# Kernel tuning notes

Hardware: AMD Instinct MI355X
Metric: run time of the kernel (lower is better)

Reference implementation:

```python
import jax, jax.numpy as jnp
import numpy as np

ALPHA = 2.0
EPS = 1e-12  # F.normalize default eps


def setup_inputs() -> dict:
    key = jax.random.key(0)
    k1, k2 = jax.random.split(key)
    x = jax.random.normal(k1, (16, 512, 48, 48), dtype=jnp.float32)
    # 1x1 conv weight [out=1, in=C, 1, 1] flattened to [C], xavier-like scale
    w_query = jax.random.normal(k2, (512,), dtype=jnp.float32) * (2.0 / (512 + 1)) ** 0.5
    return {"x": x, "w_query": w_query}


def reference(x, w_query):
    b, c, h, w = x.shape
    n = h * w
    # attention map from detached x: 1x1 conv (dot over channels) + softplus -> [b, n]
    xd = jax.lax.stop_gradient(x)
    att = jax.nn.softplus(jnp.einsum('bchw,c->bhw', xd, w_query)).reshape(b, n)
    # L2-normalize over channel dim, flatten spatial -> [b, c, n]
    norm = jnp.sqrt(jnp.sum(x * x, axis=1, keepdims=True))
    flat = (x / jnp.maximum(norm, EPS)).reshape(b, c, n)
    # full NxN similarity, relu^alpha
    sim = jnp.einsum('bcn,bcm->bnm', flat, flat)  # [b, n, n]
    score = jnp.maximum(sim, 0.0) ** ALPHA
    # combine with attention map -> refine score per spatial location
    refine = jnp.einsum('bnm,bm->bn', score, att).reshape(b, 1, h, w)
    # weighted global average pool -> [b, c, 1, 1]
    return jnp.mean(x * refine, axis=(2, 3), keepdims=True)
```

## Files before the change

### kernel.cpp

```cpp
#include <hip/hip_runtime.h>

#define C_DIM 512
#define N_PIX 2304
#define B_DIM 16
#define K8    (C_DIM / 8)
#define K8_STRIDE (N_PIX * 8)
#define FB_STRIDE ((size_t)K8 * K8_STRIDE)

typedef float floatx4 __attribute__((ext_vector_type(4)));
typedef __bf16 bf16x8 __attribute__((ext_vector_type(8)));

static __device__ __forceinline__ unsigned short f2bf(float f) {
    unsigned u = __float_as_uint(f);
    return (unsigned short)((u + 0x7fffu + ((u >> 16) & 1u)) >> 16);
}

static __device__ __forceinline__ void load_lds16(const void* g, void* l) {
    __builtin_amdgcn_global_load_lds(
        (const __attribute__((address_space(1))) unsigned int*)g,
        (__attribute__((address_space(3))) unsigned int*)l, 16, 0, 0);
}

__global__ __launch_bounds__(256) void prep_convert_kernel(const float* __restrict__ x,
                                                           const float* __restrict__ w,
                                                           float* __restrict__ rnorm,
                                                           float* __restrict__ normb,
                                                           float* __restrict__ att,
                                                           unsigned short* __restrict__ F) {
    const int tid = threadIdx.x;
    const int px = tid & 63;
    const int cc = tid >> 6;
    const int b  = (blockIdx.x * 64) / N_PIX;
    const int p0 = (blockIdx.x * 64) % N_PIX;
    const int p  = p0 + px;

    const float* xb = x + (size_t)b * C_DIM * N_PIX;

    float dot = 0.f, sq = 0.f;
    #pragma unroll 4
    for (int c = cc * 128; c < cc * 128 + 128; ++c) {
        float v = xb[(size_t)c * N_PIX + p];
        dot = fmaf(v, w[c], dot);
        sq  = fmaf(v, v, sq);
    }
    __shared__ float sdot[4][64];
    __shared__ float ssq[4][64];
    __shared__ __align__(16) float srn[64];
    sdot[cc][px] = dot;
    ssq[cc][px]  = sq;
    __syncthreads();
    if (cc == 0) {
        dot = sdot[0][px] + sdot[1][px] + sdot[2][px] + sdot[3][px];
        sq  = ssq[0][px]  + ssq[1][px]  + ssq[2][px]  + ssq[3][px];
        float z = dot;
        float sp = (z > 0.f) ? (z + log1pf(expf(-z))) : log1pf(expf(z));
        att[b * N_PIX + p] = sp;
        float nv = fmaxf(sqrtf(sq), 1e-12f);
        normb[b * N_PIX + p] = nv;
        float rv = 1.0f / nv;
        rnorm[b * N_PIX + p] = rv;
        srn[px] = rv;
    }
    __syncthreads();

    const int n4l = tid & 15;
    const int k8b = tid >> 4;
    const float4 rv4 = *(const float4*)&srn[n4l * 4];
    #pragma unroll
    for (int it = 0; it < 4; ++it) {
        const int k8 = k8b + 16 * it;
        union { unsigned short u[4][8]; int4 v[4]; } cell;
        #pragma unroll
        for (int kk = 0; kk < 8; ++kk) {
            float4 xv = *(const float4*)(xb + (size_t)(k8 * 8 + kk) * N_PIX + p0 + n4l * 4);
            cell.u[0][kk] = f2bf(xv.x * rv4.x);
            cell.u[1][kk] = f2bf(xv.y * rv4.y);
            cell.u[2][kk] = f2bf(xv.z * rv4.z);
            cell.u[3][kk] = f2bf(xv.w * rv4.w);
        }
        unsigned short* dst = F + (size_t)b * FB_STRIDE + (size_t)k8 * K8_STRIDE
                            + (size_t)(p0 + n4l * 4) * 8;
        #pragma unroll
        for (int i = 0; i < 4; ++i)
            *(int4*)(dst + i * 8) = cell.v[i];
    }
}

__global__ __launch_bounds__(256) void refine_kernel(const unsigned short* __restrict__ F,
                                                     const float* __restrict__ att,
                                                     float* __restrict__ refine) {
    const int id   = blockIdx.x;
    const int xcd  = id & 7;
    const int slot = id >> 3;
    const int hi   = (slot >= 171) ? 1 : 0;
    const int b    = xcd + 8 * hi;
    int t = slot - 171 * hi, bi = 0;
    while (t >= 18 - bi) { t -= 18 - bi; ++bi; }
    const int bj = bi + t;
    const int n0 = bi * 128;
    const int m0 = bj * 128;
    const bool mirror = (bi != bj);

    const unsigned short* Fb = F + (size_t)b * FB_STRIDE;
    const float* ab = att + b * N_PIX;

    __shared__ __align__(16) unsigned short As[8 * 128 * 8];
    __shared__ __align__(16) unsigned short Bs[8 * 128 * 8];

    const int tid  = threadIdx.x;
    const int lane = tid & 63;
    const int wave = tid >> 6;
    const int wr = wave >> 1, wc = wave & 1;
    const int quad = lane >> 4, lcol = lane & 15;

    floatx4 acc[4][4];
    #pragma unroll
    for (int i = 0; i < 4; ++i)
        #pragma unroll
        for (int j = 0; j < 4; ++j)
            acc[i][j] = (floatx4)0.f;

    for (int ck = 0; ck < 8; ++ck) {
        __syncthreads();
        #pragma unroll
        for (int h = 0; h < 2; ++h) {
            const int kbl = wave * 2 + h;
            const unsigned short* sA = Fb + (size_t)(ck * 8 + kbl) * K8_STRIDE
                                     + (size_t)n0 * 8 + lane * 8;
            const unsigned short* sB = Fb + (size_t)(ck * 8 + kbl) * K8_STRIDE
                                     + (size_t)m0 * 8 + lane * 8;
            load_lds16(sA,       &As[kbl * 1024]);
            load_lds16(sA + 512, &As[kbl * 1024 + 512]);
            load_lds16(sB,       &Bs[kbl * 1024]);
            load_lds16(sB + 512, &Bs[kbl * 1024 + 512]);
        }
        __syncthreads();

        #pragma unroll
        for (int h = 0; h < 2; ++h) {
            const int kb = h * 4 + quad;
            bf16x8 af[4], bfr[4];
            #pragma unroll
            for (int mi = 0; mi < 4; ++mi)
                af[mi] = *(const bf16x8*)&As[(kb * 128 + wr * 64 + mi * 16 + lcol) * 8];
            #pragma unroll
            for (int ni = 0; ni < 4; ++ni)
                bfr[ni] = *(const bf16x8*)&Bs[(kb * 128 + wc * 64 + ni * 16 + lcol) * 8];
            #pragma unroll
            for (int mi = 0; mi < 4; ++mi)
                #pragma unroll
                for (int ni = 0; ni < 4; ++ni)
                    acc[mi][ni] = __builtin_amdgcn_mfma_f32_16x16x32_bf16(af[mi], bfr[ni], acc[mi][ni], 0, 0, 0);
        }
    }

    float attC[4];
    #pragma unroll
    for (int ni = 0; ni < 4; ++ni)
        attC[ni] = ab[m0 + wc * 64 + ni * 16 + lcol];

    #pragma unroll
    for (int mi = 0; mi < 4; ++mi) {
        float part[4] = {0.f, 0.f, 0.f, 0.f};
        #pragma unroll
        for (int ni = 0; ni < 4; ++ni) {
            #pragma unroll
            for (int r = 0; r < 4; ++r) {
                float s = fmaxf(acc[mi][ni][r], 0.f);
                part[r] = fmaf(s * s, attC[ni], part[r]);
            }
        }
        #pragma unroll
        for (int r = 0; r < 4; ++r) {
            float v = part[r];
            v += __shfl_xor(v, 1);
            v += __shfl_xor(v, 2);
            v += __shfl_xor(v, 4);
            v += __shfl_xor(v, 8);
            if (lcol == 0)
                atomicAdd(&refine[b * N_PIX + n0 + wr * 64 + mi * 16 + quad * 4 + r], v);
        }
    }

    if (mirror) {
        float attR[4][4];
        #pragma unroll
        for (int mi = 0; mi < 4; ++mi)
            #pragma unroll
            for (int r = 0; r < 4; ++r)
                attR[mi][r] = ab[n0 + wr * 64 + mi * 16 + quad * 4 + r];

        #pragma unroll
        for (int ni = 0; ni < 4; ++ni) {
            float msum = 0.f;
            #pragma unroll
            for (int mi = 0; mi < 4; ++mi) {
                #pragma unroll
                for (int r = 0; r < 4; ++r) {
                    float s = fmaxf(acc[mi][ni][r], 0.f);
                    msum = fmaf(s * s, attR[mi][r], msum);
                }
            }
            msum += __shfl_xor(msum, 16);
            msum += __shfl_xor(msum, 32);
            if (quad == 0)
                atomicAdd(&refine[b * N_PIX + m0 + wc * 64 + ni * 16 + lcol], msum);
        }
    }
}

__global__ __launch_bounds__(256) void refine_fallback(const float* __restrict__ x,
                                                       const float* __restrict__ rnorm,
                                                       const float* __restrict__ att,
                                                       float* __restrict__ refine) {
    const int b  = blockIdx.z;
    const int n0 = blockIdx.x * 128;
    const int m0 = blockIdx.y * 128;
    const float* xb = x + (size_t)b * C_DIM * N_PIX;
    const float* rn = rnorm + b * N_PIX;
    const float* ab = att + b * N_PIX;

    __shared__ __align__(16) unsigned short As[4 * 128 * 8];
    __shared__ __align__(16) unsigned short Bs[4 * 128 * 8];

    const int tid  = threadIdx.x;
    const int nl   = tid & 127;
    const int half = tid >> 7;
    const int lane = tid & 63;
    const int wave = tid >> 6;
    const int wr = wave >> 1, wc = wave & 1;
    const int quad = lane >> 4, lcol = lane & 15;

    const float rA = rn[n0 + nl];
    const float rB = rn[m0 + nl];

    floatx4 acc[4][4];
    #pragma unroll
    for (int i = 0; i < 4; ++i)
        #pragma unroll
        for (int j = 0; j < 4; ++j)
            acc[i][j] = (floatx4)0.f;

    for (int k0 = 0; k0 < C_DIM; k0 += 32) {
        const float* xa = xb + (size_t)(k0 + half * 16) * N_PIX;
        union { unsigned short u[16]; int4 v[2]; } ta, tb;
        #pragma unroll
        for (int j = 0; j < 16; ++j) {
            float va = xa[(size_t)j * N_PIX + n0 + nl];
            float vb = xa[(size_t)j * N_PIX + m0 + nl];
            ta.u[j] = f2bf(va * rA);
            tb.u[j] = f2bf(vb * rB);
        }
        __syncthreads();
        *(int4*)&As[((half * 2 + 0) * 128 + nl) * 8] = ta.v[0];
        *(int4*)&As[((half * 2 + 1) * 128 + nl) * 8] = ta.v[1];
        *(int4*)&Bs[((half * 2 + 0) * 128 + nl) * 8] = tb.v[0];
        *(int4*)&Bs[((half * 2 + 1) * 128 + nl) * 8] = tb.v[1];
        __syncthreads();

        bf16x8 af[4], bfr[4];
        #pragma unroll
        for (int mi = 0; mi < 4; ++mi)
            af[mi] = *(const bf16x8*)&As[(quad * 128 + wr * 64 + mi * 16 + lcol) * 8];
        #pragma unroll
        for (int ni = 0; ni < 4; ++ni)
            bfr[ni] = *(const bf16x8*)&Bs[(quad * 128 + wc * 64 + ni * 16 + lcol) * 8];
        #pragma unroll
        for (int mi = 0; mi < 4; ++mi)
            #pragma unroll
            for (int ni = 0; ni < 4; ++ni)
                acc[mi][ni] = __builtin_amdgcn_mfma_f32_16x16x32_bf16(af[mi], bfr[ni], acc[mi][ni], 0, 0, 0);
    }

    float attv[4];
    #pragma unroll
    for (int ni = 0; ni < 4; ++ni)
        attv[ni] = ab[m0 + wc * 64 + ni * 16 + lcol];

    #pragma unroll
    for (int mi = 0; mi < 4; ++mi) {
        float part[4] = {0.f, 0.f, 0.f, 0.f};
        #pragma unroll
        for (int ni = 0; ni < 4; ++ni) {
            #pragma unroll
            for (int r = 0; r < 4; ++r) {
                float s = fmaxf(acc[mi][ni][r], 0.f);
                part[r] = fmaf(s * s, attv[ni], part[r]);
            }
        }
        #pragma unroll
        for (int r = 0; r < 4; ++r) {
            float v = part[r];
            v += __shfl_xor(v, 1);
            v += __shfl_xor(v, 2);
            v += __shfl_xor(v, 4);
            v += __shfl_xor(v, 8);
            if (lcol == 0)
                atomicAdd(&refine[b * N_PIX + n0 + wr * 64 + mi * 16 + quad * 4 + r], v);
        }
    }
}

__global__ __launch_bounds__(256) void pool_kernel(const unsigned short* __restrict__ F,
                                                   const float* __restrict__ refine,
                                                   const float* __restrict__ normb,
                                                   float* __restrict__ out) {
    const int lane = threadIdx.x & 63;
    const int wave = threadIdx.x >> 6;
    const int g = blockIdx.x * 4 + wave;
    const int b = g >> 6;
    const int k8 = g & 63;
    const unsigned short* Fr = F + (size_t)b * FB_STRIDE + (size_t)k8 * K8_STRIDE;
    const float* rf = refine + b * N_PIX;
    const float* nb = normb + b * N_PIX;
    float s[8] = {0.f, 0.f, 0.f, 0.f, 0.f, 0.f, 0.f, 0.f};
    #pragma unroll 4
    for (int j = 0; j < 36; ++j) {
        const int n = j * 64 + lane;
        bf16x8 fv = *(const bf16x8*)(Fr + (size_t)n * 8);
        float rr = rf[n] * nb[n];
        #pragma unroll
        for (int kk = 0; kk < 8; ++kk)
            s[kk] = fmaf((float)fv[kk], rr, s[kk]);
    }
    #pragma unroll
    for (int kk = 0; kk < 8; ++kk) {
        float v = s[kk];
        #pragma unroll
        for (int off = 32; off > 0; off >>= 1) v += __shfl_down(v, off);
        if (lane == 0) out[b * C_DIM + k8 * 8 + kk] = v * (1.0f / N_PIX);
    }
}

__global__ __launch_bounds__(256) void pool_fallback(const float* __restrict__ x,
                                                     const float* __restrict__ refine,
                                                     float* __restrict__ out) {
    const int lane = threadIdx.x & 63;
    const int wave = threadIdx.x >> 6;
    const int g = blockIdx.x * 4 + wave;
    const int b = g >> 9;
    const float4* xr = (const float4*)(x + (size_t)g * N_PIX);
    const float4* rr = (const float4*)(refine + (size_t)b * N_PIX);
    float s = 0.f;
    #pragma unroll
    for (int j = 0; j < 9; ++j) {
        float4 xv = xr[j * 64 + lane];
        float4 rv = rr[j * 64 + lane];
        s += xv.x * rv.x + xv.y * rv.y + xv.z * rv.z + xv.w * rv.w;
    }
    #pragma unroll
    for (int off = 32; off > 0; off >>= 1) s += __shfl_down(s, off);
    if (lane == 0) out[g] = s * (1.0f / N_PIX);
}

__global__ __launch_bounds__(256) void prep_kernel(const float* __restrict__ x,
                                                   const float* __restrict__ w,
                                                   float* __restrict__ rnorm,
                                                   float* __restrict__ normb,
                                                   float* __restrict__ att) {
    const int tid = threadIdx.x;
    const int px = tid & 63;
    const int cc = tid >> 6;
    const int pglob = blockIdx.x * 64 + px;
    const int b = pglob / N_PIX;
    const int p = pglob - b * N_PIX;

    const float* xb = x + (size_t)b * C_DIM * N_PIX + p;
    float dot = 0.f, sq = 0.f;
    #pragma unroll 4
    for (int c = cc * 128; c < cc * 128 + 128; ++c) {
        float v = xb[(size_t)c * N_PIX];
        dot = fmaf(v, w[c], dot);
        sq  = fmaf(v, v, sq);
    }
    __shared__ float sdot[4][64];
    __shared__ float ssq[4][64];
    sdot[cc][px] = dot;
    ssq[cc][px]  = sq;
    __syncthreads();
    if (cc == 0) {
        dot = sdot[0][px] + sdot[1][px] + sdot[2][px] + sdot[3][px];
        sq  = ssq[0][px]  + ssq[1][px]  + ssq[2][px]  + ssq[3][px];
        float z = dot;
        float sp = (z > 0.f) ? (z + log1pf(expf(-z))) : log1pf(expf(z));
        att[pglob] = sp;
        float nv = fmaxf(sqrtf(sq), 1e-12f);
        normb[pglob] = nv;
        rnorm[pglob] = 1.0f / nv;
    }
}

extern "C" void kernel_launch(void* const* d_in, const int* in_sizes, int n_in,
                              void* d_out, int out_size, void* d_ws, size_t ws_size,
                              hipStream_t stream) {
    const float* x = (const float*)d_in[0];
    const float* w = (const float*)d_in[1];
    float* rnorm  = (float*)d_ws;
    float* normb  = rnorm + B_DIM * N_PIX;
    float* att    = normb + B_DIM * N_PIX;
    float* refine = att + B_DIM * N_PIX;
    unsigned short* F = (unsigned short*)(refine + B_DIM * N_PIX);
    float* out    = (float*)d_out;

    const size_t need = (size_t)4 * B_DIM * N_PIX * 4 + (size_t)B_DIM * FB_STRIDE * 2;

    hipMemsetAsync(refine, 0, B_DIM * N_PIX * sizeof(float), stream);
    if (ws_size >= need) {
        prep_convert_kernel<<<dim3(B_DIM * N_PIX / 64), 256, 0, stream>>>(x, w, rnorm, normb, att, F);
        refine_kernel<<<dim3(171 * 16), 256, 0, stream>>>(F, att, refine);
        pool_kernel<<<dim3(B_DIM * K8 / 4), 256, 0, stream>>>(F, refine, normb, out);
    } else {
        prep_kernel<<<dim3(B_DIM * N_PIX / 64), 256, 0, stream>>>(x, w, rnorm, normb, att);
        refine_fallback<<<dim3(18, 18, B_DIM), 256, 0, stream>>>(x, rnorm, att, refine);
        pool_fallback<<<dim3(B_DIM * C_DIM / 4), 256, 0, stream>>>(x, refine, out);
    }
}
```

Measured before the change: 210.8 us.

## Fold normalization into attention weights and fuse prep into a single pass over x

```diff
diff --git a/kernel.cpp b/kernel.cpp
--- a/kernel.cpp
+++ b/kernel.cpp
@@ -15,57 +15,32 @@
     return (unsigned short)((u + 0x7fffu + ((u >> 16) & 1u)) >> 16);
 }
 
-static __device__ __forceinline__ void load_lds16(const void* g, void* l) {
+static __device__ __forceinline__ float softplus_stable(float z) {
+    return (z > 0.f) ? (z + log1pf(expf(-z))) : log1pf(expf(z));
+}
+
+static __device__ __forceinline__ void load_lds16(const void* gp, void* l) {
     __builtin_amdgcn_global_load_lds(
-        (const __attribute__((address_space(1))) unsigned int*)g,
+        (const __attribute__((address_space(1))) unsigned int*)gp,
         (__attribute__((address_space(3))) unsigned int*)l, 16, 0, 0);
 }
 
-__global__ __launch_bounds__(256) void prep_convert_kernel(const float* __restrict__ x,
-                                                           const float* __restrict__ w,
-                                                           float* __restrict__ rnorm,
-                                                           float* __restrict__ normb,
-                                                           float* __restrict__ att,
-                                                           unsigned short* __restrict__ F) {
+__global__ __launch_bounds__(256) void xcvt_kernel(const float* __restrict__ x,
+                                                   const float* __restrict__ w,
+                                                   float* __restrict__ g,
+                                                   float* __restrict__ rn2,
+                                                   float* __restrict__ refine,
+                                                   unsigned short* __restrict__ F) {
     const int tid = threadIdx.x;
-    const int px = tid & 63;
-    const int cc = tid >> 6;
     const int b  = (blockIdx.x * 64) / N_PIX;
     const int p0 = (blockIdx.x * 64) % N_PIX;
-    const int p  = p0 + px;
-
-    const float* xb = x + (size_t)b * C_DIM * N_PIX;
-
-    float dot = 0.f, sq = 0.f;
-    #pragma unroll 4
-    for (int c = cc * 128; c < cc * 128 + 128; ++c) {
-        float v = xb[(size_t)c * N_PIX + p];
-        dot = fmaf(v, w[c], dot);
-        sq  = fmaf(v, v, sq);
-    }
-    __shared__ float sdot[4][64];
-    __shared__ float ssq[4][64];
-    __shared__ __align__(16) float srn[64];
-    sdot[cc][px] = dot;
-    ssq[cc][px]  = sq;
-    __syncthreads();
-    if (cc == 0) {
-        dot = sdot[0][px] + sdot[1][px] + sdot[2][px] + sdot[3][px];
-        sq  = ssq[0][px]  + ssq[1][px]  + ssq[2][px]  + ssq[3][px];
-        float z = dot;
-        float sp = (z > 0.f) ? (z + log1pf(expf(-z))) : log1pf(expf(z));
-        att[b * N_PIX + p] = sp;
-        float nv = fmaxf(sqrtf(sq), 1e-12f);
-        normb[b * N_PIX + p] = nv;
-        float rv = 1.0f / nv;
-        rnorm[b * N_PIX + p] = rv;
-        srn[px] = rv;
-    }
-    __syncthreads();
-
     const int n4l = tid & 15;
     const int k8b = tid >> 4;
-    const float4 rv4 = *(const float4*)&srn[n4l * 4];
+
+    const float* xb = x + (size_t)b * C_DIM * N_PIX;
+    float4 dot4 = {0.f, 0.f, 0.f, 0.f};
+    float4 sq4  = {0.f, 0.f, 0.f, 0.f};
+
     #pragma unroll
     for (int it = 0; it < 4; ++it) {
         const int k8 = k8b + 16 * it;
@@ -73,10 +48,15 @@
         #pragma unroll
         for (int kk = 0; kk < 8; ++kk) {
             float4 xv = *(const float4*)(xb + (size_t)(k8 * 8 + kk) * N_PIX + p0 + n4l * 4);
-            cell.u[0][kk] = f2bf(xv.x * rv4.x);
-            cell.u[1][kk] = f2bf(xv.y * rv4.y);
-            cell.u[2][kk] = f2bf(xv.z * rv4.z);
-            cell.u[3][kk] = f2bf(xv.w * rv4.w);
+            const float wc = w[k8 * 8 + kk];
+            dot4.x = fmaf(xv.x, wc, dot4.x);  sq4.x = fmaf(xv.x, xv.x, sq4.x);
+            dot4.y = fmaf(xv.y, wc, dot4.y);  sq4.y = fmaf(xv.y, xv.y, sq4.y);
+            dot4.z = fmaf(xv.z, wc, dot4.z);  sq4.z = fmaf(xv.z, xv.z, sq4.z);
+            dot4.w = fmaf(xv.w, wc, dot4.w);  sq4.w = fmaf(xv.w, xv.w, sq4.w);
+            cell.u[0][kk] = f2bf(xv.x);
+            cell.u[1][kk] = f2bf(xv.y);
+            cell.u[2][kk] = f2bf(xv.z);
+            cell.u[3][kk] = f2bf(xv.w);
         }
         unsigned short* dst = F + (size_t)b * FB_STRIDE + (size_t)k8 * K8_STRIDE
                             + (size_t)(p0 + n4l * 4) * 8;
@@ -84,10 +64,35 @@
         for (int i = 0; i < 4; ++i)
             *(int4*)(dst + i * 8) = cell.v[i];
     }
+
+    __shared__ float4 sdot[16][16];
+    __shared__ float4 ssq[16][16];
+    sdot[k8b][n4l] = dot4;
+    ssq[k8b][n4l]  = sq4;
+    __syncthreads();
+
+    if (tid < 16) {
+        float4 d = sdot[0][tid], s = ssq[0][tid];
+        #pragma unroll
+        for (int j = 1; j < 16; ++j) {
+            float4 dj = sdot[j][tid], sj = ssq[j][tid];
+            d.x += dj.x; d.y += dj.y; d.z += dj.z; d.w += dj.w;
+            s.x += sj.x; s.y += sj.y; s.z += sj.z; s.w += sj.w;
+        }
+        float4 r2, gv;
+        r2.x = 1.0f / fmaxf(s.x, 1e-24f);  gv.x = softplus_stable(d.x) * r2.x;
+        r2.y = 1.0f / fmaxf(s.y, 1e-24f);  gv.y = softplus_stable(d.y) * r2.y;
+        r2.z = 1.0f / fmaxf(s.z, 1e-24f);  gv.z = softplus_stable(d.z) * r2.z;
+        r2.w = 1.0f / fmaxf(s.w, 1e-24f);  gv.w = softplus_stable(d.w) * r2.w;
+        const int o = b * N_PIX + p0 + tid * 4;
+        *(float4*)(g   + o) = gv;
+        *(float4*)(rn2 + o) = r2;
+        *(float4*)(refine + o) = (float4){0.f, 0.f, 0.f, 0.f};
+    }
 }
 
 __global__ __launch_bounds__(256) void refine_kernel(const unsigned short* __restrict__ F,
-                                                     const float* __restrict__ att,
+                                                     const float* __restrict__ g,
                                                      float* __restrict__ refine) {
     const int id   = blockIdx.x;
     const int xcd  = id & 7;
@@ -102,7 +107,7 @@
     const bool mirror = (bi != bj);
 
     const unsigned short* Fb = F + (size_t)b * FB_STRIDE;
-    const float* ab = att + b * N_PIX;
+    const float* gb = g + b * N_PIX;
 
     __shared__ __align__(16) unsigned short As[8 * 128 * 8];
     __shared__ __align__(16) unsigned short Bs[8 * 128 * 8];
@@ -120,20 +125,25 @@
         for (int j = 0; j < 4; ++j)
             acc[i][j] = (floatx4)0.f;
 
+    const unsigned short* pA = Fb + (size_t)(wave * 2) * K8_STRIDE + (size_t)n0 * 8 + lane * 8;
+    const unsigned short* pB = Fb + (size_t)(wave * 2) * K8_STRIDE + (size_t)m0 * 8 + lane * 8;
+    unsigned short* const lA0 = &As[(wave * 2) * 1024];
+    unsigned short* const lA1 = &As[(wave * 2 + 1) * 1024];
+    unsigned short* const lB0 = &Bs[(wave * 2) * 1024];
+    unsigned short* const lB1 = &Bs[(wave * 2 + 1) * 1024];
+
     for (int ck = 0; ck < 8; ++ck) {
         __syncthreads();
-        #pragma unroll
-        for (int h = 0; h < 2; ++h) {
-            const int kbl = wave * 2 + h;
-            const unsigned short* sA = Fb + (size_t)(ck * 8 + kbl) * K8_STRIDE
-                                     + (size_t)n0 * 8 + lane * 8;
-            const unsigned short* sB = Fb + (size_t)(ck * 8 + kbl) * K8_STRIDE
-                                     + (size_t)m0 * 8 + lane * 8;
-            load_lds16(sA,       &As[kbl * 1024]);
-            load_lds16(sA + 512, &As[kbl * 1024 + 512]);
-            load_lds16(sB,       &Bs[kbl * 1024]);
-            load_lds16(sB + 512, &Bs[kbl * 1024 + 512]);
-        }
+        load_lds16(pA,                    lA0);
+        load_lds16(pA + 512,              lA0 + 512);
+        load_lds16(pA + K8_STRIDE,        lA1);
+        load_lds16(pA + K8_STRIDE + 512,  lA1 + 512);
+        load_lds16(pB,                    lB0);
+        load_lds16(pB + 512,              lB0 + 512);
+        load_lds16(pB + K8_STRIDE,        lB1);
+        load_lds16(pB + K8_STRIDE + 512,  lB1 + 512);
+        pA += 8 * K8_STRIDE;
+        pB += 8 * K8_STRIDE;
         __syncthreads();
 
         #pragma unroll
@@ -154,10 +164,10 @@
         }
     }
 
-    float attC[4];
+    float gC[4];
     #pragma unroll
     for (int ni = 0; ni < 4; ++ni)
-        attC[ni] = ab[m0 + wc * 64 + ni * 16 + lcol];
+        gC[ni] = gb[m0 + wc * 64 + ni * 16 + lcol];
 
     #pragma unroll
     for (int mi = 0; mi < 4; ++mi) {
@@ -167,7 +177,7 @@
             #pragma unroll
             for (int r = 0; r < 4; ++r) {
                 float s = fmaxf(acc[mi][ni][r], 0.f);
-                part[r] = fmaf(s * s, attC[ni], part[r]);
+                part[r] = fmaf(s * s, gC[ni], part[r]);
             }
         }
         #pragma unroll
@@ -183,12 +193,12 @@
     }
 
     if (mirror) {
-        float attR[4][4];
+        float gR[4][4];
         #pragma unroll
         for (int mi = 0; mi < 4; ++mi)
             #pragma unroll
             for (int r = 0; r < 4; ++r)
-                attR[mi][r] = ab[n0 + wr * 64 + mi * 16 + quad * 4 + r];
+                gR[mi][r] = gb[n0 + wr * 64 + mi * 16 + quad * 4 + r];
 
         #pragma unroll
         for (int ni = 0; ni < 4; ++ni) {
@@ -198,7 +208,7 @@
                 #pragma unroll
                 for (int r = 0; r < 4; ++r) {
                     float s = fmaxf(acc[mi][ni][r], 0.f);
-                    msum = fmaf(s * s, attR[mi][r], msum);
+                    msum = fmaf(s * s, gR[mi][r], msum);
                 }
             }
             msum += __shfl_xor(msum, 16);
@@ -206,6 +216,75 @@
             if (quad == 0)
                 atomicAdd(&refine[b * N_PIX + m0 + wc * 64 + ni * 16 + lcol], msum);
         }
+    }
+}
+
+__global__ __launch_bounds__(256) void pool_kernel(const unsigned short* __restrict__ F,
+                                                   const float* __restrict__ refine,
+                                                   const float* __restrict__ rn2,
+                                                   float* __restrict__ out) {
+    const int lane = threadIdx.x & 63;
+    const int wave = threadIdx.x >> 6;
+    const int b  = blockIdx.x >> 6;
+    const int k8 = blockIdx.x & 63;
+    const unsigned short* Fr = F + (size_t)b * FB_STRIDE + (size_t)k8 * K8_STRIDE;
+    const float* rf = refine + b * N_PIX;
+    const float* r2 = rn2 + b * N_PIX;
+    float s[8] = {0.f, 0.f, 0.f, 0.f, 0.f, 0.f, 0.f, 0.f};
+    #pragma unroll
+    for (int j = 0; j < 9; ++j) {
+        const int n = (j * 4 + wave) * 64 + lane;
+        bf16x8 fv = *(const bf16x8*)(Fr + (size_t)n * 8);
+        float rr = rf[n] * r2[n];
+        #pragma unroll
+        for (int kk = 0; kk < 8; ++kk)
+            s[kk] = fmaf((float)fv[kk], rr, s[kk]);
+    }
+    __shared__ float sred[4][8];
+    #pragma unroll
+    for (int kk = 0; kk < 8; ++kk) {
+        float v = s[kk];
+        #pragma unroll
+        for (int off = 32; off > 0; off >>= 1) v += __shfl_down(v, off);
+        if (lane == 0) sred[wave][kk] = v;
+    }
+    __syncthreads();
+    if (threadIdx.x < 8) {
+        const int kk = threadIdx.x;
+        out[b * C_DIM + k8 * 8 + kk] =
+            (sred[0][kk] + sred[1][kk] + sred[2][kk] + sred[3][kk]) * (1.0f / N_PIX);
+    }
+}
+
+__global__ __launch_bounds__(256) void prep_kernel(const float* __restrict__ x,
+                                                   const float* __restrict__ w,
+                                                   float* __restrict__ rnorm,
+                                                   float* __restrict__ att) {
+    const int tid = threadIdx.x;
+    const int px = tid & 63;
+    const int cc = tid >> 6;
+    const int pglob = blockIdx.x * 64 + px;
+    const int b = pglob / N_PIX;
+    const int p = pglob - b * N_PIX;
+
+    const float* xb = x + (size_t)b * C_DIM * N_PIX + p;
+    float dot = 0.f, sq = 0.f;
+    #pragma unroll 4
+    for (int c = cc * 128; c < cc * 128 + 128; ++c) {
+        float v = xb[(size_t)c * N_PIX];
+        dot = fmaf(v, w[c], dot);
+        sq  = fmaf(v, v, sq);
+    }
+    __shared__ float sdot[4][64];
+    __shared__ float ssq[4][64];
+    sdot[cc][px] = dot;
+    ssq[cc][px]  = sq;
+    __syncthreads();
+    if (cc == 0) {
+        dot = sdot[0][px] + sdot[1][px] + sdot[2][px] + sdot[3][px];
+        sq  = ssq[0][px]  + ssq[1][px]  + ssq[2][px]  + ssq[3][px];
+        att[pglob] = softplus_stable(dot);
+        rnorm[pglob] = 1.0f / fmaxf(sqrtf(sq), 1e-12f);
     }
 }
 
@@ -301,45 +380,14 @@
     }
 }
 
-__global__ __launch_bounds__(256) void pool_kernel(const unsigned short* __restrict__ F,
-                                                   const float* __restrict__ refine,
-                                                   const float* __restrict__ normb,
-                                                   float* __restrict__ out) {
-    const int lane = threadIdx.x & 63;
-    const int wave = threadIdx.x >> 6;
-    const int g = blockIdx.x * 4 + wave;
-    const int b = g >> 6;
-    const int k8 = g & 63;
-    const unsigned short* Fr = F + (size_t)b * FB_STRIDE + (size_t)k8 * K8_STRIDE;
-    const float* rf = refine + b * N_PIX;
-    const float* nb = normb + b * N_PIX;
-    float s[8] = {0.f, 0.f, 0.f, 0.f, 0.f, 0.f, 0.f, 0.f};
-    #pragma unroll 4
-    for (int j = 0; j < 36; ++j) {
-        const int n = j * 64 + lane;
-        bf16x8 fv = *(const bf16x8*)(Fr + (size_t)n * 8);
-        float rr = rf[n] * nb[n];
-        #pragma unroll
-        for (int kk = 0; kk < 8; ++kk)
-            s[kk] = fmaf((float)fv[kk], rr, s[kk]);
-    }
-    #pragma unroll
-    for (int kk = 0; kk < 8; ++kk) {
-        float v = s[kk];
-        #pragma unroll
-        for (int off = 32; off > 0; off >>= 1) v += __shfl_down(v, off);
-        if (lane == 0) out[b * C_DIM + k8 * 8 + kk] = v * (1.0f / N_PIX);
-    }
-}
-
 __global__ __launch_bounds__(256) void pool_fallback(const float* __restrict__ x,
                                                      const float* __restrict__ refine,
                                                      float* __restrict__ out) {
     const int lane = threadIdx.x & 63;
     const int wave = threadIdx.x >> 6;
-    const int g = blockIdx.x * 4 + wave;
-    const int b = g >> 9;
-    const float4* xr = (const float4*)(x + (size_t)g * N_PIX);
+    const int gidx = blockIdx.x * 4 + wave;
+    const int b = gidx >> 9;
+    const float4* xr = (const float4*)(x + (size_t)gidx * N_PIX);
     const float4* rr = (const float4*)(refine + (size_t)b * N_PIX);
     float s = 0.f;
     #pragma unroll
@@ -350,44 +398,7 @@
     }
     #pragma unroll
     for (int off = 32; off > 0; off >>= 1) s += __shfl_down(s, off);
-    if (lane == 0) out[g] = s * (1.0f / N_PIX);
-}
-
-__global__ __launch_bounds__(256) void prep_kernel(const float* __restrict__ x,
-                                                   const float* __restrict__ w,
-                                                   float* __restrict__ rnorm,
-                                                   float* __restrict__ normb,
-                                                   float* __restrict__ att) {
-    const int tid = threadIdx.x;
-    const int px = tid & 63;
-    const int cc = tid >> 6;
-    const int pglob = blockIdx.x * 64 + px;
-    const int b = pglob / N_PIX;
-    const int p = pglob - b * N_PIX;
-
-    const float* xb = x + (size_t)b * C_DIM * N_PIX + p;
-    float dot = 0.f, sq = 0.f;
-    #pragma unroll 4
-    for (int c = cc * 128; c < cc * 128 + 128; ++c) {
-        float v = xb[(size_t)c * N_PIX];
-        dot = fmaf(v, w[c], dot);
-        sq  = fmaf(v, v, sq);
-    }
-    __shared__ float sdot[4][64];
-    __shared__ float ssq[4][64];
-    sdot[cc][px] = dot;
-    ssq[cc][px]  = sq;
-    __syncthreads();
-    if (cc == 0) {
-        dot = sdot[0][px] + sdot[1][px] + sdot[2][px] + sdot[3][px];
-        sq  = ssq[0][px]  + ssq[1][px]  + ssq[2][px]  + ssq[3][px];
-        float z = dot;
-        float sp = (z > 0.f) ? (z + log1pf(expf(-z))) : log1pf(expf(z));
-        att[pglob] = sp;
-        float nv = fmaxf(sqrtf(sq), 1e-12f);
-        normb[pglob] = nv;
-        rnorm[pglob] = 1.0f / nv;
-    }
+    if (lane == 0) out[gidx] = s * (1.0f / N_PIX);
 }
 
 extern "C" void kernel_launch(void* const* d_in, const int* in_sizes, int n_in,
@@ -395,23 +406,22 @@
                               hipStream_t stream) {
     const float* x = (const float*)d_in[0];
     const float* w = (const float*)d_in[1];
-    float* rnorm  = (float*)d_ws;
-    float* normb  = rnorm + B_DIM * N_PIX;
-    float* att    = normb + B_DIM * N_PIX;
-    float* refine = att + B_DIM * N_PIX;
+    float* rn2    = (float*)d_ws;
+    float* g      = rn2 + B_DIM * N_PIX;
+    float* refine = g + B_DIM * N_PIX;
     unsigned short* F = (unsigned short*)(refine + B_DIM * N_PIX);
     float* out    = (float*)d_out;
 
-    const size_t need = (size_t)4 * B_DIM * N_PIX * 4 + (size_t)B_DIM * FB_STRIDE * 2;
-
-    hipMemsetAsync(refine, 0, B_DIM * N_PIX * sizeof(float), stream);
+    const size_t need = (size_t)3 * B_DIM * N_PIX * 4 + (size_t)B_DIM * FB_STRIDE * 2;
+
     if (ws_size >= need) {
-        prep_convert_kernel<<<dim3(B_DIM * N_PIX / 64), 256, 0, stream>>>(x, w, rnorm, normb, att, F);
-        refine_kernel<<<dim3(171 * 16), 256, 0, stream>>>(F, att, refine);
-        pool_kernel<<<dim3(B_DIM * K8 / 4), 256, 0, stream>>>(F, refine, normb, out);
+        xcvt_kernel<<<dim3(B_DIM * N_PIX / 64), 256, 0, stream>>>(x, w, g, rn2, refine, F);
+        refine_kernel<<<dim3(171 * 16), 256, 0, stream>>>(F, g, refine);
+        pool_kernel<<<dim3(B_DIM * K8), 256, 0, stream>>>(F, refine, rn2, out);
     } else {
-        prep_kernel<<<dim3(B_DIM * N_PIX / 64), 256, 0, stream>>>(x, w, rnorm, normb, att);
-        refine_fallback<<<dim3(18, 18, B_DIM), 256, 0, stream>>>(x, rnorm, att, refine);
+        hipMemsetAsync(refine, 0, B_DIM * N_PIX * sizeof(float), stream);
+        prep_kernel<<<dim3(B_DIM * N_PIX / 64), 256, 0, stream>>>(x, w, rn2, g);
+        refine_fallback<<<dim3(18, 18, B_DIM), 256, 0, stream>>>(x, rn2, g, refine);
         pool_fallback<<<dim3(B_DIM * C_DIM / 4), 256, 0, stream>>>(x, refine, out);
     }
 }
```

Result: no change. 208.7 us (-1.0%).
